# Performance work log

Hardware: AMD Instinct MI355X
Metric: run time of the kernel (lower is better)

The kernel has to match this reference:

```python
import jax, jax.numpy as jnp
import numpy as np

L_GNN = 4          # num_layers - 1
NUM_GRAPHS = 64
BN_EPS = 1e-5


def _bn(x, g, b):
    # torch BatchNorm1d in training mode: biased variance, per-feature affine
    m = x.mean(axis=0)
    v = ((x - m) ** 2).mean(axis=0)
    return g * (x - m) * jax.lax.rsqrt(v + BN_EPS) + b


def _mlp(x, W1, b1, g, bb, W2, b2):
    # GIN 2-layer MLP: Linear -> BN -> ReLU -> Linear
    h = jax.nn.relu(_bn(x @ W1 + b1, g, bb))
    return h @ W2 + b2


def setup_inputs():
    key = jax.random.key(0)
    ks = jax.random.split(key, 20)
    N1, N2, E1, E2 = 8192, 4096, 262144, 65536
    D1, D2, H, O = 128, 64, 512, 10

    def nrm(k, shape, scale=0.05):
        return (jax.random.normal(k, shape) * scale).astype(jnp.float32)

    return {
        "x1": jax.random.normal(ks[0], (N1, D1), jnp.float32),
        "x2": jax.random.normal(ks[1], (N2, D2), jnp.float32),
        "motif2A": jax.random.uniform(ks[2], (N2, N1), jnp.float32),
        "edge1": jax.random.randint(ks[3], (2, E1), 0, N1),
        "edge2": jax.random.randint(ks[4], (2, E2), 0, N2),
        "graph_ids": jnp.sort(jax.random.randint(ks[5], (N1,), 0, NUM_GRAPHS)),
        "eps": jnp.zeros((L_GNN,), jnp.float32),
        "atts": jax.random.uniform(ks[6], (2,), jnp.float32),
        "mlp1_W1_0": nrm(ks[7], (D1, H)),
        "mlp1_W1_rest": nrm(ks[8], (L_GNN - 1, 2 * H, H)),
        "mlp1_b1": jnp.zeros((L_GNN, H), jnp.float32),
        "mlp1_bn_g": jnp.ones((L_GNN, H), jnp.float32),
        "mlp1_bn_b": jnp.zeros((L_GNN, H), jnp.float32),
        "mlp1_W2": nrm(ks[9], (L_GNN, H, H)),
        "mlp1_b2": jnp.zeros((L_GNN, H), jnp.float32),
        "bn1_g": jnp.ones((L_GNN, H), jnp.float32),
        "bn1_b": jnp.zeros((L_GNN, H), jnp.float32),
        "mlp2_W1_0": nrm(ks[10], (D2, H)),
        "mlp2_W1_rest": nrm(ks[11], (L_GNN - 1, H, H)),
        "mlp2_b1": jnp.zeros((L_GNN, H), jnp.float32),
        "mlp2_bn_g": jnp.ones((L_GNN, H), jnp.float32),
        "mlp2_bn_b": jnp.zeros((L_GNN, H), jnp.float32),
        "mlp2_W2": nrm(ks[12], (L_GNN, H, H)),
        "mlp2_b2": jnp.zeros((L_GNN, H), jnp.float32),
        "bn2_g": jnp.ones((L_GNN, H), jnp.float32),
        "bn2_b": jnp.zeros((L_GNN, H), jnp.float32),
        "pred_W0": nrm(ks[13], (D1, O)),
        "pred_b0": jnp.zeros((O,), jnp.float32),
        "pred_W": nrm(ks[14], (L_GNN, 2 * H, O)),
        "pred_b": jnp.zeros((L_GNN, O), jnp.float32),
    }


def reference(x1, x2, motif2A, edge1, edge2, graph_ids, eps, atts,
              mlp1_W1_0, mlp1_W1_rest, mlp1_b1, mlp1_bn_g, mlp1_bn_b, mlp1_W2, mlp1_b2,
              bn1_g, bn1_b,
              mlp2_W1_0, mlp2_W1_rest, mlp2_b1, mlp2_bn_g, mlp2_bn_b, mlp2_W2, mlp2_b2,
              bn2_g, bn2_b,
              pred_W0, pred_b0, pred_W, pred_b):
    N1, N2 = x1.shape[0], x2.shape[0]
    a = jax.nn.softmax(atts)                      # attention over [self-graph, hyper-graph]
    h1, h2 = x1, x2
    hidden = [x1]
    for l in range(L_GNN):
        # spmm(Adj, h) == scatter-sum of source features onto destination rows
        pooled1 = jax.ops.segment_sum(h1[edge1[1]], edge1[0], num_segments=N1)
        pooled1 = pooled1 + (1.0 + eps[l]) * h1   # learn_eps branch (next_layer_eps)
        W1 = mlp1_W1_0 if l == 0 else mlp1_W1_rest[l - 1]
        rep1 = _mlp(pooled1, W1, mlp1_b1[l], mlp1_bn_g[l], mlp1_bn_b[l], mlp1_W2[l], mlp1_b2[l])
        h1 = jax.nn.relu(_bn(rep1, bn1_g[l], bn1_b[l]))
        # hyper graph branch
        pooled2 = jax.ops.segment_sum(h2[edge2[1]], edge2[0], num_segments=N2)
        pooled2 = pooled2 + (1.0 + eps[l]) * h2
        W1h = mlp2_W1_0 if l == 0 else mlp2_W1_rest[l - 1]
        rep2 = _mlp(pooled2, W1h, mlp2_b1[l], mlp2_bn_g[l], mlp2_bn_b[l], mlp2_W2[l], mlp2_b2[l])
        h2 = jax.nn.relu(_bn(rep2, bn2_g[l], bn2_b[l]))
        # project hyper-node features back to base nodes and fuse with attention
        h2A = motif2A.T @ h2                      # [N1, H]
        h1 = jnp.concatenate([a[0] * h1, a[1] * h2A], axis=1)  # [N1, 2H]
        hidden.append(h1)
    # jumping-knowledge readout: sum graph pooling + per-layer linear heads
    score = jax.ops.segment_sum(hidden[0], graph_ids, num_segments=NUM_GRAPHS) @ pred_W0 + pred_b0
    for l in range(L_GNN):
        pooled_h = jax.ops.segment_sum(hidden[l + 1], graph_ids, num_segments=NUM_GRAPHS)
        score = score + pooled_h @ pred_W[l] + pred_b[l]
    return score
```

## Files before the change

kernel.cpp:

```cpp
#include <hip/hip_runtime.h>

using bf16x8 = __attribute__((ext_vector_type(8))) short;
using f32x4  = __attribute__((ext_vector_type(4))) float;
using u16x4  = __attribute__((ext_vector_type(4))) unsigned short;
using as3_void  = __attribute__((address_space(3))) void;
using as1_cvoid = const __attribute__((address_space(1))) void;

__device__ __forceinline__ unsigned short f2bf(float x) {
    union { float f; unsigned u; } v; v.f = x;
    unsigned r = v.u + 0x7FFFu + ((v.u >> 16) & 1u);
    return (unsigned short)(r >> 16);
}
__device__ __forceinline__ float bf2f(unsigned short h) {
    union { unsigned u; float f; } v; v.u = ((unsigned)h) << 16;
    return v.f;
}

#define GEMM_BODY(BM, A, Bt, K, KBEG, KEND)                                          \
    constexpr int WROWS = (BM) / 2;                                                  \
    constexpr int MI = WROWS / 16;                                                   \
    __shared__ __align__(16) unsigned short As[(BM) * 64];                           \
    __shared__ __align__(16) unsigned short Bs[128 * 64];                            \
    const int tid  = threadIdx.x;                                                    \
    const int lane = tid & 63, wave = tid >> 6;                                      \
    const int wr = wave >> 1, wc = wave & 1;                                         \
    const int rl = lane & 15, kg = lane >> 4;                                        \
    f32x4 acc[MI][4] = {};                                                           \
    for (int kt = (KBEG); kt < (KEND); kt += 64) {                                   \
        _Pragma("unroll")                                                            \
        for (int it = 0; it < (BM) / 32; ++it) {                                     \
            int slot = it * 256 + tid;                                               \
            int r = slot >> 3, c = slot & 7;                                         \
            int cg = c ^ (r & 7);                                                    \
            const unsigned short* ga = (A) + (size_t)(m0 + r) * (K) + (kt + cg * 8); \
            __builtin_amdgcn_global_load_lds((as1_cvoid*)ga, (as3_void*)(As + slot * 8), 16, 0, 0); \
        }                                                                            \
        _Pragma("unroll")                                                            \
        for (int it = 0; it < 4; ++it) {                                             \
            int slot = it * 256 + tid;                                               \
            int r = slot >> 3, c = slot & 7;                                         \
            int cg = c ^ (r & 7);                                                    \
            const unsigned short* gb = (Bt) + (size_t)(n0 + r) * (K) + (kt + cg * 8);\
            __builtin_amdgcn_global_load_lds((as1_cvoid*)gb, (as3_void*)(Bs + slot * 8), 16, 0, 0); \
        }                                                                            \
        __syncthreads();                                                             \
        _Pragma("unroll")                                                            \
        for (int kh = 0; kh < 2; ++kh) {                                             \
            bf16x8 a_[MI], b_[4];                                                    \
            _Pragma("unroll")                                                        \
            for (int i = 0; i < MI; ++i) {                                           \
                int ra = wr * WROWS + i * 16 + rl;                                   \
                int ca = (kh * 4 + kg) ^ (ra & 7);                                   \
                a_[i] = *reinterpret_cast<const bf16x8*>(&As[ra * 64 + ca * 8]);     \
            }                                                                        \
            _Pragma("unroll")                                                        \
            for (int j = 0; j < 4; ++j) {                                            \
                int rb = wc * 64 + j * 16 + rl;                                      \
                int cb = (kh * 4 + kg) ^ (rb & 7);                                   \
                b_[j] = *reinterpret_cast<const bf16x8*>(&Bs[rb * 64 + cb * 8]);     \
            }                                                                        \
            _Pragma("unroll")                                                        \
            for (int i = 0; i < MI; ++i)                                             \
                _Pragma("unroll")                                                    \
                for (int j = 0; j < 4; ++j)                                          \
                    acc[i][j] = __builtin_amdgcn_mfma_f32_16x16x32_bf16(a_[i], b_[j], acc[i][j], 0, 0, 0); \
        }                                                                            \
        __syncthreads();                                                             \
    }

__global__ __launch_bounds__(256) void gemm_dual(
    int nb0,
    const unsigned short* __restrict__ A0, const unsigned short* __restrict__ B0,
    int K0, unsigned short* __restrict__ C0, int os0, int oo0, float* __restrict__ st0,
    const unsigned short* __restrict__ A1, const unsigned short* __restrict__ B1,
    int K1, unsigned short* __restrict__ C1, int os1, int oo1, float* __restrict__ st1)
{
    int bx = blockIdx.x;
    const unsigned short *A, *Bt; unsigned short* Cb; float* statp;
    int K, ostride, ooff;
    if (bx < nb0) { A = A0; Bt = B0; K = K0; Cb = C0; ostride = os0; ooff = oo0; statp = st0; }
    else { bx -= nb0; A = A1; Bt = B1; K = K1; Cb = C1; ostride = os1; ooff = oo1; statp = st1; }
    const int m0 = bx * 64, n0 = blockIdx.y * 128;

    GEMM_BODY(64, A, Bt, K, 0, K)

#pragma unroll
    for (int i = 0; i < MI; ++i)
#pragma unroll
        for (int j = 0; j < 4; ++j)
#pragma unroll
            for (int e = 0; e < 4; ++e) {
                int rr = m0 + wr * WROWS + i * 16 + kg * 4 + e;
                int cc = n0 + wc * 64 + j * 16 + rl;
                Cb[(size_t)rr * ostride + ooff + cc] = f2bf(acc[i][j][e]);
            }
    if (statp) {
#pragma unroll
        for (int j = 0; j < 4; ++j) {
            float s = 0.f, q = 0.f;
#pragma unroll
            for (int i = 0; i < MI; ++i)
#pragma unroll
                for (int e = 0; e < 4; ++e) {
                    float x = acc[i][j][e];
                    s += x; q += x * x;
                }
            s += __shfl_xor(s, 16); s += __shfl_xor(s, 32);
            q += __shfl_xor(q, 16); q += __shfl_xor(q, 32);
            if (kg == 0) {
                int cc = n0 + wc * 64 + j * 16 + rl;
                atomicAdd(&statp[cc], s);
                atomicAdd(&statp[512 + cc], q);
            }
        }
    }
}

__global__ __launch_bounds__(256) void gemm_splitk(
    const unsigned short* __restrict__ A, const unsigned short* __restrict__ Bt,
    int M, int N, int K, float* __restrict__ Cp)
{
    const int m0 = blockIdx.x * 128, n0 = blockIdx.y * 128;
    const int kn = K / gridDim.z, kbeg = blockIdx.z * kn;

    GEMM_BODY(128, A, Bt, K, kbeg, kbeg + kn)

    float* dst = Cp + (size_t)blockIdx.z * M * N;
#pragma unroll
    for (int i = 0; i < MI; ++i)
#pragma unroll
        for (int j = 0; j < 4; ++j)
#pragma unroll
            for (int e = 0; e < 4; ++e) {
                int rr = m0 + wr * WROWS + i * 16 + kg * 4 + e;
                int cc = n0 + wc * 64 + j * 16 + rl;
                dst[(size_t)rr * N + cc] = acc[i][j][e];
            }
}

__global__ __launch_bounds__(128) void sumk_cvt_pool(
    const f32x4* __restrict__ P, int ks, const float* __restrict__ scalep,
    unsigned short* __restrict__ out, const int* __restrict__ gid,
    float* __restrict__ pool)
{
    const int total4 = 8192 * 128;
    float sc = *scalep;
    int c = threadIdx.x;
    int r0 = blockIdx.x * 8;
    int curg = gid[r0];
    f32x4 pacc = {};
    for (int r = 0; r < 8; ++r) {
        int row = r0 + r;
        f32x4 s = P[(size_t)row * 128 + c];
        for (int z = 1; z < ks; ++z) s += P[(size_t)z * total4 + (size_t)row * 128 + c];
        u16x4 h;
        f32x4 f;
#pragma unroll
        for (int j = 0; j < 4; ++j) { h[j] = f2bf(s[j] * sc); f[j] = bf2f(h[j]); }
        *reinterpret_cast<u16x4*>(out + (size_t)row * 1024 + 512 + c * 4) = h;
        int g = gid[row];
        if (g != curg) {
#pragma unroll
            for (int j = 0; j < 4; ++j) atomicAdd(&pool[(size_t)curg * 1024 + 512 + c * 4 + j], pacc[j]);
            pacc = {}; curg = g;
        }
        pacc += f;
    }
#pragma unroll
    for (int j = 0; j < 4; ++j) atomicAdd(&pool[(size_t)curg * 1024 + 512 + c * 4 + j], pacc[j]);
}

__global__ void csr_count2(const int* __restrict__ e1, int E1, int* __restrict__ c1,
                           const int* __restrict__ e2, int E2, int* __restrict__ c2) {
    int i = blockIdx.x * 256 + threadIdx.x;
    if (i < E1) atomicAdd(&c1[e1[i]], 1);
    else if (i < E1 + E2) atomicAdd(&c2[e2[i - E1]], 1);
}

__global__ void csr_scan2(const int* __restrict__ cnt1, int n1, int* __restrict__ offs1, int* __restrict__ cur1,
                          const int* __restrict__ cnt2, int n2, int* __restrict__ offs2, int* __restrict__ cur2) {
    const int* cnt = blockIdx.x ? cnt2 : cnt1;
    int n           = blockIdx.x ? n2 : n1;
    int* offs       = blockIdx.x ? offs2 : offs1;
    int* cursor     = blockIdx.x ? cur2 : cur1;
    __shared__ int part[1024];
    int t = threadIdx.x;
    int per = n >> 10;
    int base = t * per;
    int loc[8];
    int s = 0;
    for (int j = 0; j < per; ++j) { loc[j] = s; s += cnt[base + j]; }
    part[t] = s;
    __syncthreads();
    for (int o = 1; o < 1024; o <<= 1) {
        int v = (t >= o) ? part[t - o] : 0;
        __syncthreads();
        part[t] += v;
        __syncthreads();
    }
    int excl = (t == 0) ? 0 : part[t - 1];
    for (int j = 0; j < per; ++j) {
        int v = excl + loc[j];
        offs[base + j] = v;
        cursor[base + j] = v;
    }
    if (t == 1023) offs[n] = part[1023];
}

__global__ void csr_fill2(const int* __restrict__ e1, int E1, int* __restrict__ cur1, int* __restrict__ s1,
                          const int* __restrict__ e2, int E2, int* __restrict__ cur2, int* __restrict__ s2) {
    int i = blockIdx.x * 256 + threadIdx.x;
    if (i < E1) {
        int d = e1[i], s = e1[E1 + i];
        s1[atomicAdd(&cur1[d], 1)] = s;
    } else if (i < E1 + E2) {
        int e = i - E1;
        int d = e2[e], s = e2[E2 + e];
        s2[atomicAdd(&cur2[d], 1)] = s;
    }
}

__global__ __launch_bounds__(128) void gather2_bf16(
    const u16x4* __restrict__ Y1, const int* __restrict__ offs1, const int* __restrict__ srcs1,
    u16x4* __restrict__ T1, int n1,
    const u16x4* __restrict__ Y2, const int* __restrict__ offs2, const int* __restrict__ srcs2,
    u16x4* __restrict__ T2,
    const float* __restrict__ epsv, int l)
{
    int i = blockIdx.x;
    const u16x4* Y; u16x4* T; const int *offs, *srcs;
    if (i < n1) { Y = Y1; T = T1; offs = offs1; srcs = srcs1; }
    else        { i -= n1; Y = Y2; T = T2; offs = offs2; srcs = srcs2; }
    int c = threadIdx.x;
    float e = 1.0f + epsv[l];
    int lo = offs[i], hi = offs[i + 1];
    u16x4 hv = Y[(size_t)i * 128 + c];
    f32x4 a0, a1 = {}, a2 = {}, a3 = {};
#pragma unroll
    for (int j = 0; j < 4; ++j) a0[j] = e * bf2f(hv[j]);
    int k = lo;
    for (; k + 4 <= hi; k += 4) {
        int s0 = srcs[k], s1 = srcs[k + 1], s2 = srcs[k + 2], s3 = srcs[k + 3];
        u16x4 v0 = Y[(size_t)s0 * 128 + c];
        u16x4 v1 = Y[(size_t)s1 * 128 + c];
        u16x4 v2 = Y[(size_t)s2 * 128 + c];
        u16x4 v3 = Y[(size_t)s3 * 128 + c];
#pragma unroll
        for (int j = 0; j < 4; ++j) {
            a0[j] += bf2f(v0[j]); a1[j] += bf2f(v1[j]);
            a2[j] += bf2f(v2[j]); a3[j] += bf2f(v3[j]);
        }
    }
    for (; k < hi; ++k) {
        u16x4 v = Y[(size_t)srcs[k] * 128 + c];
#pragma unroll
        for (int j = 0; j < 4; ++j) a0[j] += bf2f(v[j]);
    }
    f32x4 acc = (a0 + a1) + (a2 + a3);
    u16x4 o;
#pragma unroll
    for (int j = 0; j < 4; ++j) o[j] = f2bf(acc[j]);
    T[(size_t)i * 128 + c] = o;
}

__global__ void bn_stats2(int nb0,
                          const u16x4* __restrict__ X0, float* __restrict__ ss0,
                          const u16x4* __restrict__ X1, float* __restrict__ ss1) {
    int bx = blockIdx.x;
    const u16x4* X; float* ss;
    if (bx < nb0) { X = X0; ss = ss0; }
    else { bx -= nb0; X = X1; ss = ss1; }
    int c = threadIdx.x;
    int r0 = bx * 16;
    f32x4 s = {}, q = {};
    for (int r = 0; r < 16; ++r) {
        u16x4 v = X[(size_t)(r0 + r) * 128 + c];
        f32x4 f;
#pragma unroll
        for (int j = 0; j < 4; ++j) f[j] = bf2f(v[j]);
        s += f; q += f * f;
    }
#pragma unroll
    for (int j = 0; j < 4; ++j) {
        atomicAdd(&ss[c * 4 + j], s[j]);
        atomicAdd(&ss[512 + c * 4 + j], q[j]);
    }
}

__global__ __launch_bounds__(128) void bn_apply2(
    int nb0, const int* __restrict__ gid,
    const u16x4* __restrict__ X0, int M0, const float* __restrict__ ss0,
    const float* __restrict__ g0, const float* __restrict__ b0,
    unsigned short* __restrict__ o0, int os0, int oo0,
    const float* __restrict__ sc0, float* __restrict__ pool0,
    const u16x4* __restrict__ X1, int M1, const float* __restrict__ ss1,
    const float* __restrict__ g1, const float* __restrict__ b1,
    unsigned short* __restrict__ o1, int os1, int oo1,
    const float* __restrict__ sc1, float* __restrict__ pool1)
{
    int bx = blockIdx.x;
    const u16x4* X; const float *ss, *g, *b, *scp; unsigned short* out;
    int M, ostride, ooff; float* pool;
    if (bx < nb0) { X = X0; M = M0; ss = ss0; g = g0; b = b0; out = o0; ostride = os0; ooff = oo0; scp = sc0; pool = pool0; }
    else { bx -= nb0; X = X1; M = M1; ss = ss1; g = g1; b = b1; out = o1; ostride = os1; ooff = oo1; scp = sc1; pool = pool1; }
    int c = threadIdx.x;
    float inv = 1.0f / (float)M;
    float al[4], be[4];
#pragma unroll
    for (int i = 0; i < 4; ++i) {
        float mean = ss[c * 4 + i] * inv;
        float var  = ss[512 + c * 4 + i] * inv - mean * mean;
        al[i] = g[c * 4 + i] * rsqrtf(var + 1e-5f);
        be[i] = b[c * 4 + i] - mean * al[i];
    }
    float sc = scp ? *scp : 1.0f;
    int r0 = bx * 8;
    int curg = pool ? gid[r0] : 0;
    f32x4 pacc = {};
    for (int r = 0; r < 8; ++r) {
        int row = r0 + r;
        u16x4 v = X[(size_t)row * 128 + c];
        u16x4 h;
        f32x4 f;
#pragma unroll
        for (int i = 0; i < 4; ++i) {
            h[i] = f2bf(fmaxf(al[i] * bf2f(v[i]) + be[i], 0.f) * sc);
            f[i] = bf2f(h[i]);
        }
        *reinterpret_cast<u16x4*>(out + (size_t)row * ostride + ooff + c * 4) = h;
        if (pool) {
            int gg = gid[row];
            if (gg != curg) {
#pragma unroll
                for (int j = 0; j < 4; ++j) atomicAdd(&pool[(size_t)curg * 1024 + ooff + c * 4 + j], pacc[j]);
                pacc = {}; curg = gg;
            }
            pacc += f;
        }
    }
    if (pool) {
#pragma unroll
        for (int j = 0; j < 4; ++j) atomicAdd(&pool[(size_t)curg * 1024 + ooff + c * 4 + j], pacc[j]);
    }
}

__global__ void cvt_bf16(const f32x4* __restrict__ X, u16x4* __restrict__ out, int n4) {
    for (int i = blockIdx.x * blockDim.x + threadIdx.x; i < n4; i += gridDim.x * blockDim.x) {
        f32x4 v = X[i];
        u16x4 h;
#pragma unroll
        for (int j = 0; j < 4; ++j) h[j] = f2bf(v[j]);
        out[i] = h;
    }
}

__global__ __launch_bounds__(256) void motif_transpose(const float* __restrict__ S,
                                                       unsigned short* __restrict__ D) {
    __shared__ unsigned short tile[64][66];
    int m0 = blockIdx.x * 64;
    int k0 = blockIdx.y * 64;
    int t = threadIdx.x;
    int r = t >> 4, cq = t & 15;
#pragma unroll
    for (int p = 0; p < 4; ++p) {
        int row = r + p * 16;
        f32x4 v = *reinterpret_cast<const f32x4*>(S + (size_t)(k0 + row) * 8192 + m0 + cq * 4);
        u16x4 h;
#pragma unroll
        for (int j = 0; j < 4; ++j) h[j] = f2bf(v[j]);
        *reinterpret_cast<u16x4*>(&tile[row][cq * 4]) = h;
    }
    __syncthreads();
#pragma unroll
    for (int p = 0; p < 4; ++p) {
        int col = r + p * 16;
        u16x4 h;
#pragma unroll
        for (int i = 0; i < 4; ++i) h[i] = tile[cq * 4 + i][col];
        *reinterpret_cast<u16x4*>(D + (size_t)(m0 + col) * 4096 + k0 + cq * 4) = h;
    }
}

__global__ void transpose_cvt_b(const float* __restrict__ S, unsigned short* __restrict__ D,
                                int rows, int cols, size_t sstride, size_t dstride) {
    S += blockIdx.z * sstride; D += blockIdx.z * dstride;
    __shared__ unsigned short tile[32][33];
    int x0 = blockIdx.x * 32, y0 = blockIdx.y * 32;
    for (int j = threadIdx.y; j < 32; j += blockDim.y)
        tile[j][threadIdx.x] = f2bf(S[(size_t)(y0 + j) * cols + x0 + threadIdx.x]);
    __syncthreads();
    for (int j = threadIdx.y; j < 32; j += blockDim.y)
        D[(size_t)(x0 + j) * rows + y0 + threadIdx.x] = tile[threadIdx.x][j];
}

__global__ void transpose_cvt11(const float* __restrict__ A, unsigned short* __restrict__ Ad,
                                const float* __restrict__ B, unsigned short* __restrict__ Bd,
                                const float* __restrict__ Cs, unsigned short* __restrict__ Cd) {
    int z = blockIdx.z;
    const float* S; unsigned short* D;
    if (z < 4)      { S = A  + (size_t)z * 262144;       D = Ad + (size_t)z * 262144; }
    else if (z < 7) { S = B  + (size_t)(z - 4) * 262144; D = Bd + (size_t)(z - 4) * 262144; }
    else            { S = Cs + (size_t)(z - 7) * 262144; D = Cd + (size_t)(z - 7) * 262144; }
    __shared__ unsigned short tile[32][33];
    int x0 = blockIdx.x * 32, y0 = blockIdx.y * 32;
    for (int j = threadIdx.y; j < 32; j += blockDim.y)
        tile[j][threadIdx.x] = f2bf(S[(size_t)(y0 + j) * 512 + x0 + threadIdx.x]);
    __syncthreads();
    for (int j = threadIdx.y; j < 32; j += blockDim.y)
        D[(size_t)(x0 + j) * 512 + y0 + threadIdx.x] = tile[threadIdx.x][j];
}

__global__ void transpose_bf16(const unsigned short* __restrict__ S, unsigned short* __restrict__ D,
                               int rows, int cols) {
    __shared__ unsigned short tile[32][33];
    int x0 = blockIdx.x * 32, y0 = blockIdx.y * 32;
    for (int j = threadIdx.y; j < 32; j += blockDim.y)
        tile[j][threadIdx.x] = S[(size_t)(y0 + j) * cols + x0 + threadIdx.x];
    __syncthreads();
    for (int j = threadIdx.y; j < 32; j += blockDim.y)
        D[(size_t)(x0 + j) * rows + y0 + threadIdx.x] = tile[threadIdx.x][j];
}

__device__ __forceinline__ int lbound(const int* __restrict__ a, int n, int v) {
    int lo = 0, hi = n;
    while (lo < hi) { int m = (lo + hi) >> 1; if (a[m] < v) lo = m + 1; else hi = m; }
    return lo;
}

__global__ void pool_f32_at(const float* __restrict__ Hm, const int* __restrict__ gid,
                            int n, float* __restrict__ P) {
    int g = blockIdx.x;
    int lo = lbound(gid, n, g), hi = lbound(gid, n, g + 1);
    int cnt = hi - lo;
    int per = (cnt + 3) >> 2;
    int s = lo + blockIdx.y * per;
    int e = min(s + per, hi);
    if (s >= e) return;
    int c = threadIdx.x;
    f32x4 acc = {};
    for (int i = s; i < e; ++i)
        acc += *reinterpret_cast<const f32x4*>(Hm + (size_t)i * 128 + c * 4);
#pragma unroll
    for (int j = 0; j < 4; ++j)
        atomicAdd(&P[(size_t)g * 128 + c * 4 + j], acc[j]);
}

__global__ void softmax2(const float* __restrict__ atts, float* __restrict__ a) {
    if (threadIdx.x == 0) {
        float m = fmaxf(atts[0], atts[1]);
        float e0 = expf(atts[0] - m), e1 = expf(atts[1] - m);
        float inv = 1.0f / (e0 + e1);
        a[0] = e0 * inv; a[1] = e1 * inv;
    }
}

__global__ __launch_bounds__(256) void score_kernel(
    const float* __restrict__ P0, const float* __restrict__ PL,
    const float* __restrict__ W0, const float* __restrict__ b0,
    const float* __restrict__ W, const float* __restrict__ bb,
    float* __restrict__ out)
{
    int g = blockIdx.x;
    int t = threadIdx.x;
    float part[10];
#pragma unroll
    for (int o = 0; o < 10; ++o) part[o] = 0.f;
    if (t < 128) {
        float p = P0[g * 128 + t];
#pragma unroll
        for (int o = 0; o < 10; ++o) part[o] += p * W0[t * 10 + o];
    }
    for (int l = 0; l < 4; ++l) {
        const float* p = PL + (size_t)l * 65536 + (size_t)g * 1024;
        const float* w = W + (size_t)l * 10240;
        for (int k = t; k < 1024; k += 256) {
            float pv = p[k];
#pragma unroll
            for (int o = 0; o < 10; ++o) part[o] += pv * w[k * 10 + o];
        }
    }
    __shared__ float red[4][10];
#pragma unroll
    for (int o = 0; o < 10; ++o) {
        float v = part[o];
        for (int off = 32; off; off >>= 1) v += __shfl_down(v, off, 64);
        if ((t & 63) == 0) red[t >> 6][o] = v;
    }
    __syncthreads();
    if (t < 10) {
        float s = b0[t] + red[0][t] + red[1][t] + red[2][t] + red[3][t];
#pragma unroll
        for (int l = 0; l < 4; ++l) s += bb[l * 10 + t];
        out[g * 10 + t] = s;
    }
}

extern "C" void kernel_launch(void* const* d_in, const int* in_sizes, int n_in,
                              void* d_out, int out_size, void* d_ws, size_t ws_size,
                              hipStream_t stream) {
    const float* x1    = (const float*)d_in[0];
    const float* x2    = (const float*)d_in[1];
    const float* motif = (const float*)d_in[2];
    const int*   edge1 = (const int*)d_in[3];
    const int*   edge2 = (const int*)d_in[4];
    const int*   gid   = (const int*)d_in[5];
    const float* epsv  = (const float*)d_in[6];
    const float* atts  = (const float*)d_in[7];
    const float* m1W10 = (const float*)d_in[8];
    const float* m1W1r = (const float*)d_in[9];
    const float* m1bng = (const float*)d_in[11];
    const float* m1bnb = (const float*)d_in[12];
    const float* m1W2  = (const float*)d_in[13];
    const float* bn1g  = (const float*)d_in[15];
    const float* bn1b  = (const float*)d_in[16];
    const float* m2W10 = (const float*)d_in[17];
    const float* m2W1r = (const float*)d_in[18];
    const float* m2bng = (const float*)d_in[20];
    const float* m2bnb = (const float*)d_in[21];
    const float* m2W2  = (const float*)d_in[22];
    const float* bn2g  = (const float*)d_in[24];
    const float* bn2b  = (const float*)d_in[25];
    const float* pW0   = (const float*)d_in[26];
    const float* pb0   = (const float*)d_in[27];
    const float* pW    = (const float*)d_in[28];
    const float* pb    = (const float*)d_in[29];
    float* out = (float*)d_out;

    constexpr int N1 = 8192, N2 = 4096, E1 = 262144, E2 = 65536;

    char* base = (char*)d_ws;
    size_t off = 0;
    auto alloc = [&](size_t bytes) -> void* {
        void* p = base + off;
        off = (off + bytes + 255) & ~(size_t)255;
        return p;
    };

    unsigned short* motifT  = (unsigned short*)alloc((size_t)8192 * 4096 * 2);
    unsigned short* w1t1_0  = (unsigned short*)alloc((size_t)512 * 128 * 2);
    unsigned short* w1t1_r  = (unsigned short*)alloc((size_t)3 * 512 * 1024 * 2);
    unsigned short* w2t1    = (unsigned short*)alloc((size_t)4 * 512 * 512 * 2);
    unsigned short* w1t2_0  = (unsigned short*)alloc((size_t)512 * 64 * 2);
    unsigned short* w1t2_r  = (unsigned short*)alloc((size_t)3 * 512 * 512 * 2);
    unsigned short* w2t2    = (unsigned short*)alloc((size_t)4 * 512 * 512 * 2);
    unsigned short* x1b     = (unsigned short*)alloc((size_t)N1 * 128 * 2);
    unsigned short* x2b     = (unsigned short*)alloc((size_t)N2 * 64 * 2);
    unsigned short* H1b     = (unsigned short*)alloc((size_t)N1 * 1024 * 2);
    unsigned short* H2b     = (unsigned short*)alloc((size_t)N2 * 512 * 2);
    unsigned short* H2t     = (unsigned short*)alloc((size_t)512 * 4096 * 2);
    unsigned short* U1b     = (unsigned short*)alloc((size_t)N1 * 512 * 2);
    unsigned short* U2b     = (unsigned short*)alloc((size_t)N2 * 512 * 2);
    unsigned short* Y1b     = (unsigned short*)alloc((size_t)N1 * 512 * 2);
    unsigned short* T1b     = (unsigned short*)alloc((size_t)N1 * 512 * 2);
    unsigned short* Y2b     = (unsigned short*)alloc((size_t)N2 * 512 * 2);
    unsigned short* T2b     = (unsigned short*)alloc((size_t)N2 * 512 * 2);
    int*   cnt1 = (int*)alloc((size_t)N1 * 4);
    int*   cnt2 = (int*)alloc((size_t)N2 * 4);
    float* ss   = (float*)alloc((size_t)16 * 1024 * 4);
    float* PL   = (float*)alloc((size_t)4 * 64 * 1024 * 4);
    float* P0   = (float*)alloc((size_t)64 * 128 * 4);
    const size_t zero_bytes = (size_t)N1 * 4 + N2 * 4 + 16 * 1024 * 4 + 4 * 64 * 1024 * 4 + 64 * 128 * 4;
    int*   offs1 = (int*)alloc((size_t)(N1 + 1) * 4);
    int*   offs2 = (int*)alloc((size_t)(N2 + 1) * 4);
    int*   cur1  = (int*)alloc((size_t)N1 * 4);
    int*   cur2  = (int*)alloc((size_t)N2 * 4);
    int*   srcs1 = (int*)alloc((size_t)E1 * 4);
    int*   srcs2 = (int*)alloc((size_t)E2 * 4);
    float* aDev  = (float*)alloc(256);

    if (off > ws_size) return;

    const size_t part_elems = (size_t)N1 * 512;
    size_t rem = ws_size - off;
    int KS = (rem >= 4 * part_elems * 4) ? 4 : (rem >= 2 * part_elems * 4) ? 2 : 1;
    float* Cpart = (float*)(base + off);

    hipMemsetAsync(cnt1, 0, zero_bytes, stream);
    softmax2<<<1, 64, 0, stream>>>(atts, aDev);
    cvt_bf16<<<512, 256, 0, stream>>>((const f32x4*)x1, (u16x4*)x1b, N1 * 128 / 4);
    cvt_bf16<<<256, 256, 0, stream>>>((const f32x4*)x2, (u16x4*)x2b, N2 * 64 / 4);
    motif_transpose<<<dim3(128, 64), 256, 0, stream>>>(motif, motifT);
    transpose_cvt_b<<<dim3(16, 4, 1), dim3(32, 8), 0, stream>>>(m1W10, w1t1_0, 128, 512, 0, 0);
    transpose_cvt_b<<<dim3(16, 32, 3), dim3(32, 8), 0, stream>>>(m1W1r, w1t1_r, 1024, 512,
                                                                 (size_t)1024 * 512, (size_t)512 * 1024);
    transpose_cvt_b<<<dim3(16, 2, 1), dim3(32, 8), 0, stream>>>(m2W10, w1t2_0, 64, 512, 0, 0);
    transpose_cvt11<<<dim3(16, 16, 11), dim3(32, 8), 0, stream>>>(m1W2, w2t1, m2W1r, w1t2_r, m2W2, w2t2);
    csr_count2<<<(E1 + E2) / 256, 256, 0, stream>>>(edge1, E1, cnt1, edge2, E2, cnt2);
    csr_scan2<<<2, 1024, 0, stream>>>(cnt1, N1, offs1, cur1, cnt2, N2, offs2, cur2);
    csr_fill2<<<(E1 + E2) / 256, 256, 0, stream>>>(edge1, E1, cur1, srcs1, edge2, E2, cur2, srcs2);
    pool_f32_at<<<dim3(64, 4), 32, 0, stream>>>(x1, gid, N1, P0);

    for (int l = 0; l < 4; ++l) {
        float* ssl = ss + (size_t)l * 4096;
        float* PLl = PL + (size_t)l * 65536;
        gemm_dual<<<dim3(192, 4), 256, 0, stream>>>(
            128,
            l ? H1b : x1b, l ? w1t1_r + (size_t)(l - 1) * 512 * 1024 : w1t1_0,
            l ? 1024 : 128, Y1b, 512, 0, nullptr,
            l ? H2b : x2b, l ? w1t2_r + (size_t)(l - 1) * 512 * 512 : w1t2_0,
            l ? 512 : 64, Y2b, 512, 0, nullptr);
        gather2_bf16<<<N1 + N2, 128, 0, stream>>>(
            (const u16x4*)Y1b, offs1, srcs1, (u16x4*)T1b, N1,
            (const u16x4*)Y2b, offs2, srcs2, (u16x4*)T2b, epsv, l);
        bn_stats2<<<768, 128, 0, stream>>>(512, (const u16x4*)T1b, ssl + 0 * 1024,
                                           (const u16x4*)T2b, ssl + 2 * 1024);
        bn_apply2<<<1536, 128, 0, stream>>>(
            1024, gid,
            (const u16x4*)T1b, N1, ssl + 0 * 1024, m1bng + l * 512, m1bnb + l * 512,
            U1b, 512, 0, nullptr, nullptr,
            (const u16x4*)T2b, N2, ssl + 2 * 1024, m2bng + l * 512, m2bnb + l * 512,
            U2b, 512, 0, nullptr, nullptr);
        gemm_dual<<<dim3(192, 4), 256, 0, stream>>>(
            128,
            U1b, w2t1 + (size_t)l * 512 * 512, 512, Y1b, 512, 0, ssl + 1 * 1024,
            U2b, w2t2 + (size_t)l * 512 * 512, 512, Y2b, 512, 0, ssl + 3 * 1024);
        bn_apply2<<<1536, 128, 0, stream>>>(
            1024, gid,
            (const u16x4*)Y1b, N1, ssl + 1 * 1024, bn1g + l * 512, bn1b + l * 512,
            H1b, 1024, 0, aDev + 0, PLl,
            (const u16x4*)Y2b, N2, ssl + 3 * 1024, bn2g + l * 512, bn2b + l * 512,
            H2b, 512, 0, nullptr, nullptr);
        transpose_bf16<<<dim3(16, 128), dim3(32, 8), 0, stream>>>(H2b, H2t, N2, 512);
        gemm_splitk<<<dim3(64, 4, KS), 256, 0, stream>>>(motifT, H2t, N1, 512, 4096, Cpart);
        sumk_cvt_pool<<<1024, 128, 0, stream>>>((const f32x4*)Cpart, KS, aDev + 1,
                                                H1b, gid, PLl);
    }

    score_kernel<<<64, 256, 0, stream>>>(P0, PL, pW0, pb0, pW, pb, out);
}
```

Measured before the change: 1.028 ms.

## Fuse BN stats into gather, fold transpose into BN apply, merge finale kernels

The gather kernel now accumulates per-feature BN sum and sum-of-squares into 64 partial slots, which removes the separate bn_stats pass over T. bn_apply_mid reduces those partials before normalizing. The hyper-branch BN apply also writes the transposed H2t directly, replacing the standalone transpose kernel. The base-branch BN apply/pool and the split-K sum/convert/pool are merged into one finale launch, and the two input conversions are combined into one launch. This cuts several launches and full-tensor passes per layer, at the cost of more atomics in gather and a 64-way partial reduction in every apply block.

```diff
diff --git a/kernel.cpp b/kernel.cpp
--- a/kernel.cpp
+++ b/kernel.cpp
@@ -3,6 +3,7 @@
 using bf16x8 = __attribute__((ext_vector_type(8))) short;
 using f32x4  = __attribute__((ext_vector_type(4))) float;
 using u16x4  = __attribute__((ext_vector_type(4))) unsigned short;
+using u16x8  = __attribute__((ext_vector_type(8))) unsigned short;
 using as3_void  = __attribute__((address_space(3))) void;
 using as1_cvoid = const __attribute__((address_space(1))) void;
 
@@ -71,15 +72,15 @@
 __global__ __launch_bounds__(256) void gemm_dual(
     int nb0,
     const unsigned short* __restrict__ A0, const unsigned short* __restrict__ B0,
-    int K0, unsigned short* __restrict__ C0, int os0, int oo0, float* __restrict__ st0,
+    int K0, unsigned short* __restrict__ C0, float* __restrict__ st0,
     const unsigned short* __restrict__ A1, const unsigned short* __restrict__ B1,
-    int K1, unsigned short* __restrict__ C1, int os1, int oo1, float* __restrict__ st1)
+    int K1, unsigned short* __restrict__ C1, float* __restrict__ st1)
 {
     int bx = blockIdx.x;
     const unsigned short *A, *Bt; unsigned short* Cb; float* statp;
-    int K, ostride, ooff;
-    if (bx < nb0) { A = A0; Bt = B0; K = K0; Cb = C0; ostride = os0; ooff = oo0; statp = st0; }
-    else { bx -= nb0; A = A1; Bt = B1; K = K1; Cb = C1; ostride = os1; ooff = oo1; statp = st1; }
+    int K;
+    if (bx < nb0) { A = A0; Bt = B0; K = K0; Cb = C0; statp = st0; }
+    else { bx -= nb0; A = A1; Bt = B1; K = K1; Cb = C1; statp = st1; }
     const int m0 = bx * 64, n0 = blockIdx.y * 128;
 
     GEMM_BODY(64, A, Bt, K, 0, K)
@@ -92,7 +93,7 @@
             for (int e = 0; e < 4; ++e) {
                 int rr = m0 + wr * WROWS + i * 16 + kg * 4 + e;
                 int cc = n0 + wc * 64 + j * 16 + rl;
-                Cb[(size_t)rr * ostride + ooff + cc] = f2bf(acc[i][j][e]);
+                Cb[(size_t)rr * 512 + cc] = f2bf(acc[i][j][e]);
             }
     if (statp) {
 #pragma unroll
@@ -136,38 +137,6 @@
                 int cc = n0 + wc * 64 + j * 16 + rl;
                 dst[(size_t)rr * N + cc] = acc[i][j][e];
             }
-}
-
-__global__ __launch_bounds__(128) void sumk_cvt_pool(
-    const f32x4* __restrict__ P, int ks, const float* __restrict__ scalep,
-    unsigned short* __restrict__ out, const int* __restrict__ gid,
-    float* __restrict__ pool)
-{
-    const int total4 = 8192 * 128;
-    float sc = *scalep;
-    int c = threadIdx.x;
-    int r0 = blockIdx.x * 8;
-    int curg = gid[r0];
-    f32x4 pacc = {};
-    for (int r = 0; r < 8; ++r) {
-        int row = r0 + r;
-        f32x4 s = P[(size_t)row * 128 + c];
-        for (int z = 1; z < ks; ++z) s += P[(size_t)z * total4 + (size_t)row * 128 + c];
-        u16x4 h;
-        f32x4 f;
-#pragma unroll
-        for (int j = 0; j < 4; ++j) { h[j] = f2bf(s[j] * sc); f[j] = bf2f(h[j]); }
-        *reinterpret_cast<u16x4*>(out + (size_t)row * 1024 + 512 + c * 4) = h;
-        int g = gid[row];
-        if (g != curg) {
-#pragma unroll
-            for (int j = 0; j < 4; ++j) atomicAdd(&pool[(size_t)curg * 1024 + 512 + c * 4 + j], pacc[j]);
-            pacc = {}; curg = g;
-        }
-        pacc += f;
-    }
-#pragma unroll
-    for (int j = 0; j < 4; ++j) atomicAdd(&pool[(size_t)curg * 1024 + 512 + c * 4 + j], pacc[j]);
 }
 
 __global__ void csr_count2(const int* __restrict__ e1, int E1, int* __restrict__ c1,
@@ -222,15 +191,15 @@
 
 __global__ __launch_bounds__(128) void gather2_bf16(
     const u16x4* __restrict__ Y1, const int* __restrict__ offs1, const int* __restrict__ srcs1,
-    u16x4* __restrict__ T1, int n1,
+    u16x4* __restrict__ T1, int n1, float* __restrict__ ssp1,
     const u16x4* __restrict__ Y2, const int* __restrict__ offs2, const int* __restrict__ srcs2,
-    u16x4* __restrict__ T2,
+    u16x4* __restrict__ T2, float* __restrict__ ssp2,
     const float* __restrict__ epsv, int l)
 {
     int i = blockIdx.x;
-    const u16x4* Y; u16x4* T; const int *offs, *srcs;
-    if (i < n1) { Y = Y1; T = T1; offs = offs1; srcs = srcs1; }
-    else        { i -= n1; Y = Y2; T = T2; offs = offs2; srcs = srcs2; }
+    const u16x4* Y; u16x4* T; const int *offs, *srcs; float* ssp;
+    if (i < n1) { Y = Y1; T = T1; offs = offs1; srcs = srcs1; ssp = ssp1; }
+    else        { i -= n1; Y = Y2; T = T2; offs = offs2; srcs = srcs2; ssp = ssp2; }
     int c = threadIdx.x;
     float e = 1.0f + epsv[l];
     int lo = offs[i], hi = offs[i + 1];
@@ -258,51 +227,61 @@
     }
     f32x4 acc = (a0 + a1) + (a2 + a3);
     u16x4 o;
-#pragma unroll
-    for (int j = 0; j < 4; ++j) o[j] = f2bf(acc[j]);
+    f32x4 f;
+#pragma unroll
+    for (int j = 0; j < 4; ++j) { o[j] = f2bf(acc[j]); f[j] = bf2f(o[j]); }
     T[(size_t)i * 128 + c] = o;
-}
-
-__global__ void bn_stats2(int nb0,
-                          const u16x4* __restrict__ X0, float* __restrict__ ss0,
-                          const u16x4* __restrict__ X1, float* __restrict__ ss1) {
-    int bx = blockIdx.x;
-    const u16x4* X; float* ss;
-    if (bx < nb0) { X = X0; ss = ss0; }
-    else { bx -= nb0; X = X1; ss = ss1; }
-    int c = threadIdx.x;
-    int r0 = bx * 16;
-    f32x4 s = {}, q = {};
-    for (int r = 0; r < 16; ++r) {
-        u16x4 v = X[(size_t)(r0 + r) * 128 + c];
-        f32x4 f;
-#pragma unroll
-        for (int j = 0; j < 4; ++j) f[j] = bf2f(v[j]);
-        s += f; q += f * f;
-    }
+    float* sp = ssp + (size_t)(blockIdx.x & 63) * 1024;
 #pragma unroll
     for (int j = 0; j < 4; ++j) {
-        atomicAdd(&ss[c * 4 + j], s[j]);
-        atomicAdd(&ss[512 + c * 4 + j], q[j]);
-    }
-}
-
-__global__ __launch_bounds__(128) void bn_apply2(
-    int nb0, const int* __restrict__ gid,
-    const u16x4* __restrict__ X0, int M0, const float* __restrict__ ss0,
-    const float* __restrict__ g0, const float* __restrict__ b0,
-    unsigned short* __restrict__ o0, int os0, int oo0,
-    const float* __restrict__ sc0, float* __restrict__ pool0,
-    const u16x4* __restrict__ X1, int M1, const float* __restrict__ ss1,
-    const float* __restrict__ g1, const float* __restrict__ b1,
-    unsigned short* __restrict__ o1, int os1, int oo1,
-    const float* __restrict__ sc1, float* __restrict__ pool1)
+        atomicAdd(&sp[c * 4 + j], f[j]);
+        atomicAdd(&sp[512 + c * 4 + j], f[j] * f[j]);
+    }
+}
+
+__global__ __launch_bounds__(128) void bn_apply_mid(
+    int nb0,
+    const u16x4* __restrict__ X0, int M0, const float* __restrict__ ssp0,
+    const float* __restrict__ g0, const float* __restrict__ b0, unsigned short* __restrict__ o0,
+    const u16x4* __restrict__ X1, int M1, const float* __restrict__ ssp1,
+    const float* __restrict__ g1, const float* __restrict__ b1, unsigned short* __restrict__ o1)
 {
     int bx = blockIdx.x;
-    const u16x4* X; const float *ss, *g, *b, *scp; unsigned short* out;
-    int M, ostride, ooff; float* pool;
-    if (bx < nb0) { X = X0; M = M0; ss = ss0; g = g0; b = b0; out = o0; ostride = os0; ooff = oo0; scp = sc0; pool = pool0; }
-    else { bx -= nb0; X = X1; M = M1; ss = ss1; g = g1; b = b1; out = o1; ostride = os1; ooff = oo1; scp = sc1; pool = pool1; }
+    const u16x4* X; const float *ssp, *g, *b; unsigned short* out; int M;
+    if (bx < nb0) { X = X0; M = M0; ssp = ssp0; g = g0; b = b0; out = o0; }
+    else { bx -= nb0; X = X1; M = M1; ssp = ssp1; g = g1; b = b1; out = o1; }
+    int c = threadIdx.x;
+    f32x4 s = {}, q = {};
+#pragma unroll 8
+    for (int p = 0; p < 64; ++p) {
+        s += *reinterpret_cast<const f32x4*>(ssp + (size_t)p * 1024 + c * 4);
+        q += *reinterpret_cast<const f32x4*>(ssp + (size_t)p * 1024 + 512 + c * 4);
+    }
+    float inv = 1.0f / (float)M;
+    float al[4], be[4];
+#pragma unroll
+    for (int i = 0; i < 4; ++i) {
+        float mean = s[i] * inv;
+        float var  = q[i] * inv - mean * mean;
+        al[i] = g[c * 4 + i] * rsqrtf(var + 1e-5f);
+        be[i] = b[c * 4 + i] - mean * al[i];
+    }
+    int r0 = bx * 8;
+    for (int r = 0; r < 8; ++r) {
+        u16x4 v = X[(size_t)(r0 + r) * 128 + c];
+        u16x4 h;
+#pragma unroll
+        for (int i = 0; i < 4; ++i)
+            h[i] = f2bf(fmaxf(al[i] * bf2f(v[i]) + be[i], 0.f));
+        *reinterpret_cast<u16x4*>(out + (size_t)(r0 + r) * 512 + c * 4) = h;
+    }
+}
+
+__global__ __launch_bounds__(128) void bn_apply_b2t(
+    const u16x4* __restrict__ X, int M, const float* __restrict__ ss,
+    const float* __restrict__ g, const float* __restrict__ b,
+    unsigned short* __restrict__ out, unsigned short* __restrict__ outT)
+{
     int c = threadIdx.x;
     float inv = 1.0f / (float)M;
     float al[4], be[4];
@@ -313,44 +292,98 @@
         al[i] = g[c * 4 + i] * rsqrtf(var + 1e-5f);
         be[i] = b[c * 4 + i] - mean * al[i];
     }
-    float sc = scp ? *scp : 1.0f;
+    int r0 = blockIdx.x * 8;
+    u16x8 t8[4];
+#pragma unroll
+    for (int r = 0; r < 8; ++r) {
+        u16x4 v = X[(size_t)(r0 + r) * 128 + c];
+        u16x4 h;
+#pragma unroll
+        for (int i = 0; i < 4; ++i) {
+            h[i] = f2bf(fmaxf(al[i] * bf2f(v[i]) + be[i], 0.f));
+            t8[i][r] = h[i];
+        }
+        *reinterpret_cast<u16x4*>(out + (size_t)(r0 + r) * 512 + c * 4) = h;
+    }
+#pragma unroll
+    for (int i = 0; i < 4; ++i)
+        *reinterpret_cast<u16x8*>(outT + (size_t)(c * 4 + i) * 4096 + r0) = t8[i];
+}
+
+__global__ __launch_bounds__(128) void finale(
+    int nb0, const int* __restrict__ gid, const float* __restrict__ aDev,
+    float* __restrict__ pool, unsigned short* __restrict__ H1,
+    const u16x4* __restrict__ X, const float* __restrict__ ss,
+    const float* __restrict__ g, const float* __restrict__ b,
+    const f32x4* __restrict__ P, int ks)
+{
+    int bx = blockIdx.x;
+    int c = threadIdx.x;
+    int job = bx >= nb0;
+    if (job) bx -= nb0;
     int r0 = bx * 8;
-    int curg = pool ? gid[r0] : 0;
+    int ooff = job ? 512 : 0;
+    float al[4], be[4];
+    float sc;
+    if (!job) {
+        sc = aDev[0];
+        float inv = 1.0f / 8192.0f;
+#pragma unroll
+        for (int i = 0; i < 4; ++i) {
+            float mean = ss[c * 4 + i] * inv;
+            float var  = ss[512 + c * 4 + i] * inv - mean * mean;
+            al[i] = g[c * 4 + i] * rsqrtf(var + 1e-5f);
+            be[i] = b[c * 4 + i] - mean * al[i];
+        }
+    } else {
+        sc = aDev[1];
+    }
+    const int total4 = 8192 * 128;
+    int curg = gid[r0];
     f32x4 pacc = {};
     for (int r = 0; r < 8; ++r) {
         int row = r0 + r;
-        u16x4 v = X[(size_t)row * 128 + c];
         u16x4 h;
         f32x4 f;
-#pragma unroll
-        for (int i = 0; i < 4; ++i) {
-            h[i] = f2bf(fmaxf(al[i] * bf2f(v[i]) + be[i], 0.f) * sc);
-            f[i] = bf2f(h[i]);
+        if (!job) {
+            u16x4 v = X[(size_t)row * 128 + c];
+#pragma unroll
+            for (int i = 0; i < 4; ++i) {
+                h[i] = f2bf(fmaxf(al[i] * bf2f(v[i]) + be[i], 0.f) * sc);
+                f[i] = bf2f(h[i]);
+            }
+        } else {
+            f32x4 s = P[(size_t)row * 128 + c];
+            for (int z = 1; z < ks; ++z) s += P[(size_t)z * total4 + (size_t)row * 128 + c];
+#pragma unroll
+            for (int i = 0; i < 4; ++i) { h[i] = f2bf(s[i] * sc); f[i] = bf2f(h[i]); }
         }
-        *reinterpret_cast<u16x4*>(out + (size_t)row * ostride + ooff + c * 4) = h;
-        if (pool) {
-            int gg = gid[row];
-            if (gg != curg) {
-#pragma unroll
-                for (int j = 0; j < 4; ++j) atomicAdd(&pool[(size_t)curg * 1024 + ooff + c * 4 + j], pacc[j]);
-                pacc = {}; curg = gg;
-            }
-            pacc += f;
+        *reinterpret_cast<u16x4*>(H1 + (size_t)row * 1024 + ooff + c * 4) = h;
+        int gg = gid[row];
+        if (gg != curg) {
+#pragma unroll
+            for (int j = 0; j < 4; ++j)
+                atomicAdd(&pool[(size_t)curg * 1024 + ooff + c * 4 + j], pacc[j]);
+            pacc = {}; curg = gg;
         }
-    }
-    if (pool) {
-#pragma unroll
-        for (int j = 0; j < 4; ++j) atomicAdd(&pool[(size_t)curg * 1024 + ooff + c * 4 + j], pacc[j]);
-    }
-}
-
-__global__ void cvt_bf16(const f32x4* __restrict__ X, u16x4* __restrict__ out, int n4) {
-    for (int i = blockIdx.x * blockDim.x + threadIdx.x; i < n4; i += gridDim.x * blockDim.x) {
-        f32x4 v = X[i];
+        pacc += f;
+    }
+#pragma unroll
+    for (int j = 0; j < 4; ++j)
+        atomicAdd(&pool[(size_t)curg * 1024 + ooff + c * 4 + j], pacc[j]);
+}
+
+__global__ void cvt2_bf16(const f32x4* __restrict__ X0, u16x4* __restrict__ O0, int n0,
+                          const f32x4* __restrict__ X1, u16x4* __restrict__ O1, int n1) {
+    for (int i = blockIdx.x * blockDim.x + threadIdx.x; i < n0 + n1; i += gridDim.x * blockDim.x) {
+        const f32x4* X; u16x4* O; int k;
+        if (i < n0) { X = X0; O = O0; k = i; }
+        else { X = X1; O = O1; k = i - n0; }
+        f32x4 v = X[k];
         u16x4 h;
 #pragma unroll
         for (int j = 0; j < 4; ++j) h[j] = f2bf(v[j]);
-        out[i] = h;
+        O[k] = h;
     }
 }
 
@@ -408,17 +441,6 @@
     __syncthreads();
     for (int j = threadIdx.y; j < 32; j += blockDim.y)
         D[(size_t)(x0 + j) * 512 + y0 + threadIdx.x] = tile[threadIdx.x][j];
-}
-
-__global__ void transpose_bf16(const unsigned short* __restrict__ S, unsigned short* __restrict__ D,
-                               int rows, int cols) {
-    __shared__ unsigned short tile[32][33];
-    int x0 = blockIdx.x * 32, y0 = blockIdx.y * 32;
-    for (int j = threadIdx.y; j < 32; j += blockDim.y)
-        tile[j][threadIdx.x] = S[(size_t)(y0 + j) * cols + x0 + threadIdx.x];
-    __syncthreads();
-    for (int j = threadIdx.y; j < 32; j += blockDim.y)
-        D[(size_t)(x0 + j) * rows + y0 + threadIdx.x] = tile[threadIdx.x][j];
 }
 
 __device__ __forceinline__ int lbound(const int* __restrict__ a, int n, int v) {
@@ -559,7 +581,10 @@
     float* ss   = (float*)alloc((size_t)16 * 1024 * 4);
     float* PL   = (float*)alloc((size_t)4 * 64 * 1024 * 4);
     float* P0   = (float*)alloc((size_t)64 * 128 * 4);
-    const size_t zero_bytes = (size_t)N1 * 4 + N2 * 4 + 16 * 1024 * 4 + 4 * 64 * 1024 * 4 + 64 * 128 * 4;
+    float* ssp1 = (float*)alloc((size_t)4 * 64 * 1024 * 4);
+    float* ssp2 = (float*)alloc((size_t)4 * 64 * 1024 * 4);
+    const size_t zero_bytes = (size_t)N1 * 4 + N2 * 4 + 16 * 1024 * 4 + 4 * 64 * 1024 * 4
+                            + 64 * 128 * 4 + 2 * (size_t)4 * 64 * 1024 * 4;
     int*   offs1 = (int*)alloc((size_t)(N1 + 1) * 4);
     int*   offs2 = (int*)alloc((size_t)(N2 + 1) * 4);
     int*   cur1  = (int*)alloc((size_t)N1 * 4);
@@ -577,8 +602,8 @@
 
     hipMemsetAsync(cnt1, 0, zero_bytes, stream);
     softmax2<<<1, 64, 0, stream>>>(atts, aDev);
-    cvt_bf16<<<512, 256, 0, stream>>>((const f32x4*)x1, (u16x4*)x1b, N1 * 128 / 4);
-    cvt_bf16<<<256, 256, 0, stream>>>((const f32x4*)x2, (u16x4*)x2b, N2 * 64 / 4);
+    cvt2_bf16<<<512, 256, 0, stream>>>((const f32x4*)x1, (u16x4*)x1b, N1 * 128 / 4,
+                                       (const f32x4*)x2, (u16x4*)x2b, N2 * 64 / 4);
     motif_transpose<<<dim3(128, 64), 256, 0, stream>>>(motif, motifT);
     transpose_cvt_b<<<dim3(16, 4, 1), dim3(32, 8), 0, stream>>>(m1W10, w1t1_0, 128, 512, 0, 0);
     transpose_cvt_b<<<dim3(16, 32, 3), dim3(32, 8), 0, stream>>>(m1W1r, w1t1_r, 1024, 512,
@@ -591,39 +616,34 @@
     pool_f32_at<<<dim3(64, 4), 32, 0, stream>>>(x1, gid, N1, P0);
 
     for (int l = 0; l < 4; ++l) {
-        float* ssl = ss + (size_t)l * 4096;
-        float* PLl = PL + (size_t)l * 65536;
+        float* ssl   = ss + (size_t)l * 4096;
+        float* PLl   = PL + (size_t)l * 65536;
+        float* ssp1l = ssp1 + (size_t)l * 65536;
+        float* ssp2l = ssp2 + (size_t)l * 65536;
         gemm_dual<<<dim3(192, 4), 256, 0, stream>>>(
             128,
             l ? H1b : x1b, l ? w1t1_r + (size_t)(l - 1) * 512 * 1024 : w1t1_0,
-            l ? 1024 : 128, Y1b, 512, 0, nullptr,
+            l ? 1024 : 128, Y1b, nullptr,
             l ? H2b : x2b, l ? w1t2_r + (size_t)(l - 1) * 512 * 512 : w1t2_0,
-            l ? 512 : 64, Y2b, 512, 0, nullptr);
+            l ? 512 : 64, Y2b, nullptr);
         gather2_bf16<<<N1 + N2, 128, 0, stream>>>(
-            (const u16x4*)Y1b, offs1, srcs1, (u16x4*)T1b, N1,
-            (const u16x4*)Y2b, offs2, srcs2, (u16x4*)T2b, epsv, l);
-        bn_stats2<<<768, 128, 0, stream>>>(512, (const u16x4*)T1b, ssl + 0 * 1024,
-                                           (const u16x4*)T2b, ssl + 2 * 1024);
-        bn_apply2<<<1536, 128, 0, stream>>>(
-            1024, gid,
-            (const u16x4*)T1b, N1, ssl + 0 * 1024, m1bng + l * 512, m1bnb + l * 512,
-            U1b, 512, 0, nullptr, nullptr,
-            (const u16x4*)T2b, N2, ssl + 2 * 1024, m2bng + l * 512, m2bnb + l * 512,
-            U2b, 512, 0, nullptr, nullptr);
+            (const u16x4*)Y1b, offs1, srcs1, (u16x4*)T1b, N1, ssp1l,
+            (const u16x4*)Y2b, offs2, srcs2, (u16x4*)T2b, ssp2l, epsv, l);
+        bn_apply_mid<<<1536, 128, 0, stream>>>(
+            1024,
+            (const u16x4*)T1b, N1, ssp1l, m1bng + l * 512, m1bnb + l * 512, U1b,
+            (const u16x4*)T2b, N2, ssp2l, m2bng + l * 512, m2bnb + l * 512, U2b);
         gemm_dual<<<dim3(192, 4), 256, 0, stream>>>(
             128,
-            U1b, w2t1 + (size_t)l * 512 * 512, 512, Y1b, 512, 0, ssl + 1 * 1024,
-            U2b, w2t2 + (size_t)l * 512 * 512, 512, Y2b, 512, 0, ssl + 3 * 1024);
-        bn_apply2<<<1536, 128, 0, stream>>>(
-            1024, gid,
-            (const u16x4*)Y1b, N1, ssl + 1 * 1024, bn1g + l * 512, bn1b + l * 512,
-            H1b, 1024, 0, aDev + 0, PLl,
-            (const u16x4*)Y2b, N2, ssl + 3 * 1024, bn2g + l * 512, bn2b + l * 512,
-            H2b, 512, 0, nullptr, nullptr);
-        transpose_bf16<<<dim3(16, 128), dim3(32, 8), 0, stream>>>(H2b, H2t, N2, 512);
+            U1b, w2t1 + (size_t)l * 512 * 512, 512, Y1b, ssl + 1 * 1024,
+            U2b, w2t2 + (size_t)l * 512 * 512, 512, Y2b, ssl + 3 * 1024);
+        bn_apply_b2t<<<512, 128, 0, stream>>>(
+            (const u16x4*)Y2b, N2, ssl + 3 * 1024, bn2g + l * 512, bn2b + l * 512, H2b, H2t);
         gemm_splitk<<<dim3(64, 4, KS), 256, 0, stream>>>(motifT, H2t, N1, 512, 4096, Cpart);
-        sumk_cvt_pool<<<1024, 128, 0, stream>>>((const f32x4*)Cpart, KS, aDev + 1,
-                                                H1b, gid, PLl);
+        finale<<<2048, 128, 0, stream>>>(
+            1024, gid, aDev, PLl, H1b,
+            (const u16x4*)Y1b, ssl + 1 * 1024, bn1g + l * 512, bn1b + l * 512,
+            (const f32x4*)Cpart, KS);
     }
 
     score_kernel<<<64, 256, 0, stream>>>(P0, PL, pW0, pb0, pW, pb, out);
```

Result: slower. 1.615 ms (+57.0%).
